# Optimization experiments

Hardware: AMD Instinct MI355X
Metric: run time of the kernel (lower is better)

Reference implementation:

```python
import jax, jax.numpy as jnp
import numpy as np

D = 256          # in_dim == out_dim for both layers
B, S = 8, 1024   # batch, seq_len
EPS = 1e-5       # LayerNorm eps (torch default)


def _layernorm(x, g, b):
    mu = jnp.mean(x, axis=-1, keepdims=True)
    var = jnp.var(x, axis=-1, keepdims=True)
    return (x - mu) * jax.lax.rsqrt(var + EPS) * g + b


def _periods(d):
    i = jnp.arange(d, dtype=jnp.float32)
    # periods[i, j] = i*d + j + 2
    return i[:, None] * d + i[None, :] + 2.0


def _layer(x, M, P, g, b, positions):
    # x: [B, S, in_dim] -> [B, S, out_dim]
    x_trans = jnp.einsum('bsj,ij->bsi', x, M)      # x @ M.T
    x_trans = _layernorm(x_trans, g, b)
    k = positions.astype(jnp.float32)[:, None, None]            # [S,1,1]
    phi = jnp.cos(2.0 * jnp.pi * k / _periods(D)[None])         # [S,D,D]
    Mk = P[None] * phi                                          # [S,D,D]
    Nk = jnp.einsum('bsj,sij->bsi', x_trans, Mk)
    # use_residual='separate' with in_dim==out_dim -> Identity residual
    return Nk + x


def setup_inputs() -> dict:
    key = jax.random.key(0)
    ks = jax.random.split(key, 5)
    seq = jax.random.normal(ks[0], (B, S, D), dtype=jnp.float32)
    M1 = jax.random.uniform(ks[1], (D, D), jnp.float32, -0.5, 0.5)
    P1 = jax.random.uniform(ks[2], (D, D), jnp.float32, -0.1, 0.1)
    M2 = jax.random.uniform(ks[3], (D, D), jnp.float32, -0.5, 0.5)
    P2 = jax.random.uniform(ks[4], (D, D), jnp.float32, -0.1, 0.1)
    g1 = jnp.ones((D,), jnp.float32); b1 = jnp.zeros((D,), jnp.float32)
    g2 = jnp.ones((D,), jnp.float32); b2 = jnp.zeros((D,), jnp.float32)
    return {"seq": seq, "M1": M1, "P1": P1, "g1": g1, "b1": b1,
            "M2": M2, "P2": P2, "g2": g2, "b2": b2}


def reference(seq, M1, P1, g1, b1, M2, P2, g2, b2):
    positions = jnp.arange(S)
    x = _layer(seq, M1, P1, g1, b1, positions)
    x = _layer(x, M2, P2, g2, b2, positions)
    return x
```

## Files before the change

### kernel.cpp

```cpp
#include <hip/hip_runtime.h>

#define DD 256
#define BB 8
#define SS 1024
#define XSTRIDE 264

#define LAYER_BYTES 524288
#define PTAB_OFF    131072
#define ITAB_OFF    262144
#define WS_NEEDED   (2 * LAYER_BYTES)

typedef _Float16 half8  __attribute__((ext_vector_type(8)));
typedef _Float16 half2t __attribute__((ext_vector_type(2)));
typedef __fp16   fp16x2 __attribute__((ext_vector_type(2)));
typedef __attribute__((ext_vector_type(4))) float float4v;

__device__ __forceinline__ half2t pkrtz(float a, float b) {
    union { fp16x2 f; half2t h; } cv;
    cv.f = __builtin_amdgcn_cvt_pkrtz(a, b);
    return cv.h;
}

__global__ void build_tabs(const float* __restrict__ M1, const float* __restrict__ P1,
                           const float* __restrict__ M2, const float* __restrict__ P2,
                           char* __restrict__ ws)
{
    int gid   = blockIdx.x * 256 + threadIdx.x;
    int layer = gid >> 13;
    int gi    = gid & 8191;
    int idx   = gi >> 6;
    int lane  = gi & 63;
    int kt    = idx >> 4;
    int wt    = idx & 15;
    int l15   = lane & 15, quad = lane >> 4;
    int n     = 16 * wt + l15;
    int j0    = kt * 32 + quad * 8;

    const float* Msrc = layer ? M2 : M1;
    const float* Psrc = layer ? P2 : P1;

    union { half8 h; half2t h2[4]; } mh, ph;
    float iv[8];
    #pragma unroll
    for (int e = 0; e < 4; ++e) {
        float ma = Msrc[(size_t)n * DD + j0 + 2 * e];
        float mb = Msrc[(size_t)n * DD + j0 + 2 * e + 1];
        float pa = Psrc[(size_t)n * DD + j0 + 2 * e];
        float pb = Psrc[(size_t)n * DD + j0 + 2 * e + 1];
        mh.h2[e] = pkrtz(ma, mb);
        ph.h2[e] = pkrtz(pa, pb);
        iv[2 * e]     = 1.0f / (float)(n * DD + j0 + 2 * e + 2);
        iv[2 * e + 1] = 1.0f / (float)(n * DD + j0 + 2 * e + 3);
    }
    char* base = ws + (size_t)layer * LAYER_BYTES;
    ((half8*)base)[gi]                       = mh.h;
    ((half8*)(base + PTAB_OFF))[gi]          = ph.h;
    float4* it = (float4*)(base + ITAB_OFF);
    it[2 * gi]     = make_float4(iv[0], iv[1], iv[2], iv[3]);
    it[2 * gi + 1] = make_float4(iv[4], iv[5], iv[6], iv[7]);
}

template<bool TABS>
__global__ __launch_bounds__(512, 4)
void fused_hierddpm(const float* __restrict__ seq,
                    const float* __restrict__ M1, const float* __restrict__ P1,
                    const float* __restrict__ g1, const float* __restrict__ be1,
                    const float* __restrict__ M2, const float* __restrict__ P2,
                    const float* __restrict__ g2, const float* __restrict__ be2,
                    const char* __restrict__ ws,
                    float* __restrict__ out)
{
    __shared__ __align__(16) _Float16 xsb[16][XSTRIDE];
    __shared__ __align__(16) _Float16 xtb[16][XSTRIDE];
    __shared__ float stats[8][16][2];

    const int tid  = threadIdx.x;
    const int w    = tid >> 6;
    const int lane = tid & 63;
    const int l15  = lane & 15;
    const int quad = lane >> 4;
    const int s0   = blockIdx.x * 2;
    const float k0 = (float)s0, k1 = (float)(s0 + 1);

    {
        const float4* seq4 = (const float4*)seq;
        #pragma unroll
        for (int u = 0; u < 2; ++u) {
            int v  = tid + 512 * u;
            int sl = v >> 9;
            int rm = v & 511;
            int b  = rm >> 6, j4 = rm & 63;
            float4 x = seq4[((size_t)b * SS + s0 + sl) * 64 + j4];
            half2t* dst = (half2t*)&xsb[sl * 8 + b][4 * j4];
            dst[0] = pkrtz(x.x, x.y);
            dst[1] = pkrtz(x.z, x.w);
        }
    }

    float res[2][4];
    {
        const int sl = quad >> 1;
        #pragma unroll
        for (int t = 0; t < 2; ++t) {
            int col = 16 * (2 * w + t) + l15;
            #pragma unroll
            for (int reg = 0; reg < 4; ++reg) {
                int b = (quad * 4 + reg) & 7;
                res[t][reg] = seq[((size_t)b * SS + s0 + sl) * DD + col];
            }
        }
    }
    __syncthreads();

    #pragma unroll 1
    for (int layer = 0; layer < 2; ++layer) {
        const float* M  = layer ? M2  : M1;
        const float* P  = layer ? P2  : P1;
        const float* g  = layer ? g2  : g1;
        const float* be = layer ? be2 : be1;
        const char*  lbase = ws + (size_t)layer * LAYER_BYTES;
        const half8*  Mtab = (const half8*)lbase;
        const half8*  Ptab = (const half8*)(lbase + PTAB_OFF);
        const float4* Itab = (const float4*)(lbase + ITAB_OFF);

        float4v acc1[2];
        acc1[0] = (float4v){0.f, 0.f, 0.f, 0.f};
        acc1[1] = (float4v){0.f, 0.f, 0.f, 0.f};

        #pragma unroll 1
        for (int kt = 0; kt < 8; ++kt) {
            half8 a = *(const half8*)&xsb[l15][kt * 32 + quad * 8];
            #pragma unroll
            for (int t = 0; t < 2; ++t) {
                half8 bfrag;
                if (TABS) {
                    bfrag = Mtab[(kt * 16 + 2 * w + t) * 64 + lane];
                } else {
                    int n = 16 * (2 * w + t) + l15;
                    const float4* Mr = (const float4*)M +
                        ((size_t)n * 64 + kt * 8 + quad * 2);
                    float4 m0 = Mr[0], m1 = Mr[1];
                    union { half8 h; half2t h2[4]; } bb;
                    bb.h2[0] = pkrtz(m0.x, m0.y);
                    bb.h2[1] = pkrtz(m0.z, m0.w);
                    bb.h2[2] = pkrtz(m1.x, m1.y);
                    bb.h2[3] = pkrtz(m1.z, m1.w);
                    bfrag = bb.h;
                }
                acc1[t] = __builtin_amdgcn_mfma_f32_16x16x32_f16(a, bfrag, acc1[t], 0, 0, 0);
            }
        }

        {
            #pragma unroll
            for (int reg = 0; reg < 4; ++reg) {
                float sm = acc1[0][reg] + acc1[1][reg];
                float sq = fmaf(acc1[0][reg], acc1[0][reg], acc1[1][reg] * acc1[1][reg]);
                #pragma unroll
                for (int off = 1; off < 16; off <<= 1) {
                    sm += __shfl_xor(sm, off, 64);
                    sq += __shfl_xor(sq, off, 64);
                }
                if (l15 == 0) {
                    stats[w][quad * 4 + reg][0] = sm;
                    stats[w][quad * 4 + reg][1] = sq;
                }
            }
        }
        __syncthreads();
        {
            float mu[4], rs[4];
            #pragma unroll
            for (int reg = 0; reg < 4; ++reg) {
                int m = quad * 4 + reg;
                float sm = 0.f, sq = 0.f;
                #pragma unroll
                for (int ww = 0; ww < 8; ++ww) {
                    sm += stats[ww][m][0];
                    sq += stats[ww][m][1];
                }
                float mm = sm * (1.f / DD);
                mu[reg] = mm;
                rs[reg] = rsqrtf(sq * (1.f / DD) - mm * mm + 1e-5f);
            }
            #pragma unroll
            for (int t = 0; t < 2; ++t) {
                int col = 16 * (2 * w + t) + l15;
                float gv = g[col], bv = be[col];
                #pragma unroll
                for (int reg = 0; reg < 4; ++reg) {
                    float v = fmaf((acc1[t][reg] - mu[reg]) * rs[reg], gv, bv);
                    xtb[quad * 4 + reg][col] = (_Float16)v;
                }
            }
        }
        __syncthreads();

        float4v accS[2][2];
        #pragma unroll
        for (int sl = 0; sl < 2; ++sl)
            #pragma unroll
            for (int t = 0; t < 2; ++t) accS[sl][t] = (float4v){0.f, 0.f, 0.f, 0.f};

        #pragma unroll 2
        for (int kt = 0; kt < 8; ++kt) {
            half8 a = *(const half8*)&xtb[l15][kt * 32 + quad * 8];
            #pragma unroll
            for (int t = 0; t < 2; ++t) {
                union { half8 h; half2t h2[4]; } pv;
                float iv[8];
                if (TABS) {
                    int gi = (kt * 16 + 2 * w + t) * 64 + lane;
                    pv.h = Ptab[gi];
                    float4 i0 = Itab[2 * gi], i1 = Itab[2 * gi + 1];
                    iv[0] = i0.x; iv[1] = i0.y; iv[2] = i0.z; iv[3] = i0.w;
                    iv[4] = i1.x; iv[5] = i1.y; iv[6] = i1.z; iv[7] = i1.w;
                } else {
                    int n = 16 * (2 * w + t) + l15;
                    const float4* Pr = (const float4*)P +
                        ((size_t)n * 64 + kt * 8 + quad * 2);
                    float4 p0 = Pr[0], p1 = Pr[1];
                    pv.h2[0] = pkrtz(p0.x, p0.y);
                    pv.h2[1] = pkrtz(p0.z, p0.w);
                    pv.h2[2] = pkrtz(p1.x, p1.y);
                    pv.h2[3] = pkrtz(p1.z, p1.w);
                    float pbase = (float)(n * DD + kt * 32 + quad * 8 + 2);
                    #pragma unroll
                    for (int e = 0; e < 8; ++e)
                        iv[e] = __builtin_amdgcn_rcpf(pbase + (float)e);
                }
                union { half8 h; half2t h2[4]; } b0, b1;
                #pragma unroll
                for (int e = 0; e < 4; ++e) {
                    float ia = iv[2 * e], ib = iv[2 * e + 1];
                    half2t c0 = pkrtz(
                        __builtin_amdgcn_cosf(__builtin_amdgcn_fractf(k0 * ia)),
                        __builtin_amdgcn_cosf(__builtin_amdgcn_fractf(k0 * ib)));
                    half2t c1 = pkrtz(
                        __builtin_amdgcn_cosf(__builtin_amdgcn_fractf(k1 * ia)),
                        __builtin_amdgcn_cosf(__builtin_amdgcn_fractf(k1 * ib)));
                    b0.h2[e] = pv.h2[e] * c0;
                    b1.h2[e] = pv.h2[e] * c1;
                }
                accS[0][t] = __builtin_amdgcn_mfma_f32_16x16x32_f16(a, b0.h, accS[0][t], 0, 0, 0);
                accS[1][t] = __builtin_amdgcn_mfma_f32_16x16x32_f16(a, b1.h, accS[1][t], 0, 0, 0);
            }
        }

        #pragma unroll
        for (int t = 0; t < 2; ++t) {
            int col = 16 * (2 * w + t) + l15;
            float4v av = (quad < 2) ? accS[0][t] : accS[1][t];
            int sl = quad >> 1;
            #pragma unroll
            for (int reg = 0; reg < 4; ++reg) {
                int m = quad * 4 + reg;
                int b = m & 7;
                float val = av[reg] + res[t][reg];
                if (layer == 0) {
                    res[t][reg] = val;
                    xsb[m][col] = (_Float16)val;
                } else {
                    out[((size_t)b * SS + s0 + sl) * DD + col] = val;
                }
            }
        }
        if (layer == 0) __syncthreads();
    }
}

extern "C" void kernel_launch(void* const* d_in, const int* in_sizes, int n_in,
                              void* d_out, int out_size, void* d_ws, size_t ws_size,
                              hipStream_t stream)
{
    const float* seq = (const float*)d_in[0];
    const float* M1  = (const float*)d_in[1];
    const float* P1  = (const float*)d_in[2];
    const float* g1  = (const float*)d_in[3];
    const float* b1  = (const float*)d_in[4];
    const float* M2  = (const float*)d_in[5];
    const float* P2  = (const float*)d_in[6];
    const float* g2  = (const float*)d_in[7];
    const float* b2  = (const float*)d_in[8];
    float* out = (float*)d_out;

    if (ws_size >= WS_NEEDED) {
        build_tabs<<<64, 256, 0, stream>>>(M1, P1, M2, P2, (char*)d_ws);
        fused_hierddpm<true><<<SS / 2, 512, 0, stream>>>(
            seq, M1, P1, g1, b1, M2, P2, g2, b2, (const char*)d_ws, out);
    } else {
        fused_hierddpm<false><<<SS / 2, 512, 0, stream>>>(
            seq, M1, P1, g1, b1, M2, P2, g2, b2, nullptr, out);
    }
}
```

Baseline: 114.0 us.

## Use 1024-thread blocks with one column tile per wave and prefetch operands

```diff
diff --git a/kernel.cpp b/kernel.cpp
--- a/kernel.cpp
+++ b/kernel.cpp
@@ -61,7 +61,7 @@
 }
 
 template<bool TABS>
-__global__ __launch_bounds__(512, 4)
+__global__ __launch_bounds__(1024, 8)
 void fused_hierddpm(const float* __restrict__ seq,
                     const float* __restrict__ M1, const float* __restrict__ P1,
                     const float* __restrict__ g1, const float* __restrict__ be1,
@@ -72,7 +72,7 @@
 {
     __shared__ __align__(16) _Float16 xsb[16][XSTRIDE];
     __shared__ __align__(16) _Float16 xtb[16][XSTRIDE];
-    __shared__ float stats[8][16][2];
+    __shared__ float2 stats[16][16];
 
     const int tid  = threadIdx.x;
     const int w    = tid >> 6;
@@ -81,34 +81,24 @@
     const int quad = lane >> 4;
     const int s0   = blockIdx.x * 2;
     const float k0 = (float)s0, k1 = (float)(s0 + 1);
+    const int col  = 16 * w + l15;
 
     {
         const float4* seq4 = (const float4*)seq;
-        #pragma unroll
-        for (int u = 0; u < 2; ++u) {
-            int v  = tid + 512 * u;
-            int sl = v >> 9;
-            int rm = v & 511;
-            int b  = rm >> 6, j4 = rm & 63;
-            float4 x = seq4[((size_t)b * SS + s0 + sl) * 64 + j4];
-            half2t* dst = (half2t*)&xsb[sl * 8 + b][4 * j4];
-            dst[0] = pkrtz(x.x, x.y);
-            dst[1] = pkrtz(x.z, x.w);
-        }
-    }
-
-    float res[2][4];
-    {
-        const int sl = quad >> 1;
-        #pragma unroll
-        for (int t = 0; t < 2; ++t) {
-            int col = 16 * (2 * w + t) + l15;
-            #pragma unroll
-            for (int reg = 0; reg < 4; ++reg) {
-                int b = (quad * 4 + reg) & 7;
-                res[t][reg] = seq[((size_t)b * SS + s0 + sl) * DD + col];
-            }
-        }
+        int sl = tid >> 9;
+        int rm = tid & 511;
+        int b  = rm >> 6, j4 = rm & 63;
+        float4 x = seq4[((size_t)b * SS + s0 + sl) * 64 + j4];
+        half2t* dst = (half2t*)&xsb[sl * 8 + b][4 * j4];
+        dst[0] = pkrtz(x.x, x.y);
+        dst[1] = pkrtz(x.z, x.w);
+    }
+
+    float res[4];
+    #pragma unroll
+    for (int reg = 0; reg < 4; ++reg) {
+        int m = quad * 4 + reg;
+        res[reg] = seq[((size_t)(m & 7) * SS + s0 + (m >> 3)) * DD + col];
     }
     __syncthreads();
 
@@ -123,111 +113,85 @@
         const half8*  Ptab = (const half8*)(lbase + PTAB_OFF);
         const float4* Itab = (const float4*)(lbase + ITAB_OFF);
 
-        float4v acc1[2];
-        acc1[0] = (float4v){0.f, 0.f, 0.f, 0.f};
-        acc1[1] = (float4v){0.f, 0.f, 0.f, 0.f};
-
-        #pragma unroll 1
-        for (int kt = 0; kt < 8; ++kt) {
-            half8 a = *(const half8*)&xsb[l15][kt * 32 + quad * 8];
+        float4v acc1 = (float4v){0.f, 0.f, 0.f, 0.f};
+
+        if (TABS) {
+            half8 aN = *(const half8*)&xsb[l15][quad * 8];
+            half8 bN = Mtab[w * 64 + lane];
+            #pragma unroll 1
+            for (int kt = 0; kt < 8; ++kt) {
+                half8 aC = aN, bC = bN;
+                if (kt < 7) {
+                    aN = *(const half8*)&xsb[l15][(kt + 1) * 32 + quad * 8];
+                    bN = Mtab[((kt + 1) * 16 + w) * 64 + lane];
+                }
+                acc1 = __builtin_amdgcn_mfma_f32_16x16x32_f16(aC, bC, acc1, 0, 0, 0);
+            }
+        } else {
+            #pragma unroll 1
+            for (int kt = 0; kt < 8; ++kt) {
+                half8 a = *(const half8*)&xsb[l15][kt * 32 + quad * 8];
+                int n = 16 * w + l15;
+                const float4* Mr = (const float4*)M + ((size_t)n * 64 + kt * 8 + quad * 2);
+                float4 m0 = Mr[0], m1 = Mr[1];
+                union { half8 h; half2t h2[4]; } bb2;
+                bb2.h2[0] = pkrtz(m0.x, m0.y);
+                bb2.h2[1] = pkrtz(m0.z, m0.w);
+                bb2.h2[2] = pkrtz(m1.x, m1.y);
+                bb2.h2[3] = pkrtz(m1.z, m1.w);
+                acc1 = __builtin_amdgcn_mfma_f32_16x16x32_f16(a, bb2.h, acc1, 0, 0, 0);
+            }
+        }
+
+        #pragma unroll
+        for (int reg = 0; reg < 4; ++reg) {
+            float sm = acc1[reg];
+            float sq = acc1[reg] * acc1[reg];
             #pragma unroll
-            for (int t = 0; t < 2; ++t) {
-                half8 bfrag;
-                if (TABS) {
-                    bfrag = Mtab[(kt * 16 + 2 * w + t) * 64 + lane];
-                } else {
-                    int n = 16 * (2 * w + t) + l15;
-                    const float4* Mr = (const float4*)M +
-                        ((size_t)n * 64 + kt * 8 + quad * 2);
-                    float4 m0 = Mr[0], m1 = Mr[1];
-                    union { half8 h; half2t h2[4]; } bb;
-                    bb.h2[0] = pkrtz(m0.x, m0.y);
-                    bb.h2[1] = pkrtz(m0.z, m0.w);
-                    bb.h2[2] = pkrtz(m1.x, m1.y);
-                    bb.h2[3] = pkrtz(m1.z, m1.w);
-                    bfrag = bb.h;
-                }
-                acc1[t] = __builtin_amdgcn_mfma_f32_16x16x32_f16(a, bfrag, acc1[t], 0, 0, 0);
-            }
-        }
-
-        {
-            #pragma unroll
-            for (int reg = 0; reg < 4; ++reg) {
-                float sm = acc1[0][reg] + acc1[1][reg];
-                float sq = fmaf(acc1[0][reg], acc1[0][reg], acc1[1][reg] * acc1[1][reg]);
-                #pragma unroll
-                for (int off = 1; off < 16; off <<= 1) {
-                    sm += __shfl_xor(sm, off, 64);
-                    sq += __shfl_xor(sq, off, 64);
-                }
-                if (l15 == 0) {
-                    stats[w][quad * 4 + reg][0] = sm;
-                    stats[w][quad * 4 + reg][1] = sq;
-                }
-            }
+            for (int off = 1; off < 16; off <<= 1) {
+                sm += __shfl_xor(sm, off, 64);
+                sq += __shfl_xor(sq, off, 64);
+            }
+            if (l15 == 0) stats[w][quad * 4 + reg] = make_float2(sm, sq);
         }
         __syncthreads();
         {
-            float mu[4], rs[4];
+            float gv = g[col], bv = be[col];
             #pragma unroll
             for (int reg = 0; reg < 4; ++reg) {
                 int m = quad * 4 + reg;
                 float sm = 0.f, sq = 0.f;
                 #pragma unroll
-                for (int ww = 0; ww < 8; ++ww) {
-                    sm += stats[ww][m][0];
-                    sq += stats[ww][m][1];
+                for (int ww = 0; ww < 16; ++ww) {
+                    float2 v = stats[ww][m];
+                    sm += v.x; sq += v.y;
                 }
                 float mm = sm * (1.f / DD);
-                mu[reg] = mm;
-                rs[reg] = rsqrtf(sq * (1.f / DD) - mm * mm + 1e-5f);
-            }
-            #pragma unroll
-            for (int t = 0; t < 2; ++t) {
-                int col = 16 * (2 * w + t) + l15;
-                float gv = g[col], bv = be[col];
-                #pragma unroll
-                for (int reg = 0; reg < 4; ++reg) {
-                    float v = fmaf((acc1[t][reg] - mu[reg]) * rs[reg], gv, bv);
-                    xtb[quad * 4 + reg][col] = (_Float16)v;
-                }
+                float rs = rsqrtf(sq * (1.f / DD) - mm * mm + 1e-5f);
+                xtb[m][col] = (_Float16)fmaf((acc1[reg] - mm) * rs, gv, bv);
             }
         }
         __syncthreads();
 
-        float4v accS[2][2];
-        #pragma unroll
-        for (int sl = 0; sl < 2; ++sl)
-            #pragma unroll
-            for (int t = 0; t < 2; ++t) accS[sl][t] = (float4v){0.f, 0.f, 0.f, 0.f};
-
-        #pragma unroll 2
-        for (int kt = 0; kt < 8; ++kt) {
-            half8 a = *(const half8*)&xtb[l15][kt * 32 + quad * 8];
-            #pragma unroll
-            for (int t = 0; t < 2; ++t) {
-                union { half8 h; half2t h2[4]; } pv;
-                float iv[8];
-                if (TABS) {
-                    int gi = (kt * 16 + 2 * w + t) * 64 + lane;
-                    pv.h = Ptab[gi];
-                    float4 i0 = Itab[2 * gi], i1 = Itab[2 * gi + 1];
-                    iv[0] = i0.x; iv[1] = i0.y; iv[2] = i0.z; iv[3] = i0.w;
-                    iv[4] = i1.x; iv[5] = i1.y; iv[6] = i1.z; iv[7] = i1.w;
-                } else {
-                    int n = 16 * (2 * w + t) + l15;
-                    const float4* Pr = (const float4*)P +
-                        ((size_t)n * 64 + kt * 8 + quad * 2);
-                    float4 p0 = Pr[0], p1 = Pr[1];
-                    pv.h2[0] = pkrtz(p0.x, p0.y);
-                    pv.h2[1] = pkrtz(p0.z, p0.w);
-                    pv.h2[2] = pkrtz(p1.x, p1.y);
-                    pv.h2[3] = pkrtz(p1.z, p1.w);
-                    float pbase = (float)(n * DD + kt * 32 + quad * 8 + 2);
-                    #pragma unroll
-                    for (int e = 0; e < 8; ++e)
-                        iv[e] = __builtin_amdgcn_rcpf(pbase + (float)e);
+        float4v accS0 = (float4v){0.f, 0.f, 0.f, 0.f};
+        float4v accS1 = (float4v){0.f, 0.f, 0.f, 0.f};
+
+        if (TABS) {
+            int gi0 = w * 64 + lane;
+            half8 aN = *(const half8*)&xtb[l15][quad * 8];
+            half8 pN = Ptab[gi0];
+            float4 iN0 = Itab[2 * gi0], iN1 = Itab[2 * gi0 + 1];
+            #pragma unroll 1
+            for (int kt = 0; kt < 8; ++kt) {
+                half8 aC = aN;
+                union { half8 h; half2t h2[4]; } pv; pv.h = pN;
+                float iv[8] = {iN0.x, iN0.y, iN0.z, iN0.w, iN1.x, iN1.y, iN1.z, iN1.w};
+                if (kt < 7) {
+                    int gin = ((kt + 1) * 16 + w) * 64 + lane;
+                    aN  = *(const half8*)&xtb[l15][(kt + 1) * 32 + quad * 8];
+                    pN  = Ptab[gin];
+                    iN0 = Itab[2 * gin];
+                    iN1 = Itab[2 * gin + 1];
                 }
                 union { half8 h; half2t h2[4]; } b0, b1;
                 #pragma unroll
@@ -242,27 +206,50 @@
                     b0.h2[e] = pv.h2[e] * c0;
                     b1.h2[e] = pv.h2[e] * c1;
                 }
-                accS[0][t] = __builtin_amdgcn_mfma_f32_16x16x32_f16(a, b0.h, accS[0][t], 0, 0, 0);
-                accS[1][t] = __builtin_amdgcn_mfma_f32_16x16x32_f16(a, b1.h, accS[1][t], 0, 0, 0);
+                accS0 = __builtin_amdgcn_mfma_f32_16x16x32_f16(aC, b0.h, accS0, 0, 0, 0);
+                accS1 = __builtin_amdgcn_mfma_f32_16x16x32_f16(aC, b1.h, accS1, 0, 0, 0);
+            }
+        } else {
+            #pragma unroll 1
+            for (int kt = 0; kt < 8; ++kt) {
+                half8 a = *(const half8*)&xtb[l15][kt * 32 + quad * 8];
+                int n = 16 * w + l15;
+                const float4* Pr = (const float4*)P + ((size_t)n * 64 + kt * 8 + quad * 2);
+                float4 p0 = Pr[0], p1 = Pr[1];
+                union { half8 h; half2t h2[4]; } pv;
+                pv.h2[0] = pkrtz(p0.x, p0.y);
+                pv.h2[1] = pkrtz(p0.z, p0.w);
+                pv.h2[2] = pkrtz(p1.x, p1.y);
+                pv.h2[3] = pkrtz(p1.z, p1.w);
+                float pbase = (float)(n * DD + kt * 32 + quad * 8 + 2);
+                union { half8 h; half2t h2[4]; } b0, b1;
+                #pragma unroll
+                for (int e = 0; e < 4; ++e) {
+                    float ia = __builtin_amdgcn_rcpf(pbase + (float)(2 * e));
+                    float ib = __builtin_amdgcn_rcpf(pbase + (float)(2 * e + 1));
+                    half2t c0 = pkrtz(
+                        __builtin_amdgcn_cosf(__builtin_amdgcn_fractf(k0 * ia)),
+                        __builtin_amdgcn_cosf(__builtin_amdgcn_fractf(k0 * ib)));
+                    half2t c1 = pkrtz(
+                        __builtin_amdgcn_cosf(__builtin_amdgcn_fractf(k1 * ia)),
+                        __builtin_amdgcn_cosf(__builtin_amdgcn_fractf(k1 * ib)));
+                    b0.h2[e] = pv.h2[e] * c0;
+                    b1.h2[e] = pv.h2[e] * c1;
+                }
+                accS0 = __builtin_amdgcn_mfma_f32_16x16x32_f16(a, b0.h, accS0, 0, 0, 0);
+                accS1 = __builtin_amdgcn_mfma_f32_16x16x32_f16(a, b1.h, accS1, 0, 0, 0);
             }
         }
 
         #pragma unroll
-        for (int t = 0; t < 2; ++t) {
-            int col = 16 * (2 * w + t) + l15;
-            float4v av = (quad < 2) ? accS[0][t] : accS[1][t];
-            int sl = quad >> 1;
-            #pragma unroll
-            for (int reg = 0; reg < 4; ++reg) {
-                int m = quad * 4 + reg;
-                int b = m & 7;
-                float val = av[reg] + res[t][reg];
-                if (layer == 0) {
-                    res[t][reg] = val;
-                    xsb[m][col] = (_Float16)val;
-                } else {
-                    out[((size_t)b * SS + s0 + sl) * DD + col] = val;
-                }
+        for (int reg = 0; reg < 4; ++reg) {
+            int m = quad * 4 + reg;
+            float av = ((quad < 2) ? accS0[reg] : accS1[reg]) + res[reg];
+            if (layer == 0) {
+                res[reg] = av;
+                xsb[m][col] = (_Float16)av;
+            } else {
+                out[((size_t)(m & 7) * SS + s0 + (m >> 3)) * DD + col] = av;
             }
         }
         if (layer == 0) __syncthreads();
@@ -286,10 +273,10 @@
 
     if (ws_size >= WS_NEEDED) {
         build_tabs<<<64, 256, 0, stream>>>(M1, P1, M2, P2, (char*)d_ws);
-        fused_hierddpm<true><<<SS / 2, 512, 0, stream>>>(
+        fused_hierddpm<true><<<SS / 2, 1024, 0, stream>>>(
             seq, M1, P1, g1, b1, M2, P2, g2, b2, (const char*)d_ws, out);
     } else {
-        fused_hierddpm<false><<<SS / 2, 512, 0, stream>>>(
+        fused_hierddpm<false><<<SS / 2, 1024, 0, stream>>>(
             seq, M1, P1, g1, b1, M2, P2, g2, b2, nullptr, out);
     }
 }
```

Measured after the change: 177.8 us. +56.0%, slower.

## Split batch across two blocks per position pair and recompute reciprocal periods inline

Applied to the files above, without the earlier changes.

```diff
diff --git a/kernel.cpp b/kernel.cpp
--- a/kernel.cpp
+++ b/kernel.cpp
@@ -5,9 +5,8 @@
 #define SS 1024
 #define XSTRIDE 264
 
-#define LAYER_BYTES 524288
+#define LAYER_BYTES 262144
 #define PTAB_OFF    131072
-#define ITAB_OFF    262144
 #define WS_NEEDED   (2 * LAYER_BYTES)
 
 typedef _Float16 half8  __attribute__((ext_vector_type(8)));
@@ -30,9 +29,9 @@
     int gi    = gid & 8191;
     int idx   = gi >> 6;
     int lane  = gi & 63;
-    int kt    = idx >> 4;
     int wt    = idx & 15;
     int l15   = lane & 15, quad = lane >> 4;
+    int kt    = idx >> 4;
     int n     = 16 * wt + l15;
     int j0    = kt * 32 + quad * 8;
 
@@ -40,7 +39,6 @@
     const float* Psrc = layer ? P2 : P1;
 
     union { half8 h; half2t h2[4]; } mh, ph;
-    float iv[8];
     #pragma unroll
     for (int e = 0; e < 4; ++e) {
         float ma = Msrc[(size_t)n * DD + j0 + 2 * e];
@@ -49,19 +47,14 @@
         float pb = Psrc[(size_t)n * DD + j0 + 2 * e + 1];
         mh.h2[e] = pkrtz(ma, mb);
         ph.h2[e] = pkrtz(pa, pb);
-        iv[2 * e]     = 1.0f / (float)(n * DD + j0 + 2 * e + 2);
-        iv[2 * e + 1] = 1.0f / (float)(n * DD + j0 + 2 * e + 3);
     }
     char* base = ws + (size_t)layer * LAYER_BYTES;
-    ((half8*)base)[gi]                       = mh.h;
-    ((half8*)(base + PTAB_OFF))[gi]          = ph.h;
-    float4* it = (float4*)(base + ITAB_OFF);
-    it[2 * gi]     = make_float4(iv[0], iv[1], iv[2], iv[3]);
-    it[2 * gi + 1] = make_float4(iv[4], iv[5], iv[6], iv[7]);
+    ((half8*)base)[gi]              = mh.h;
+    ((half8*)(base + PTAB_OFF))[gi] = ph.h;
 }
 
 template<bool TABS>
-__global__ __launch_bounds__(512, 4)
+__global__ __launch_bounds__(512, 6)
 void fused_hierddpm(const float* __restrict__ seq,
                     const float* __restrict__ M1, const float* __restrict__ P1,
                     const float* __restrict__ g1, const float* __restrict__ be1,
@@ -72,42 +65,38 @@
 {
     __shared__ __align__(16) _Float16 xsb[16][XSTRIDE];
     __shared__ __align__(16) _Float16 xtb[16][XSTRIDE];
-    __shared__ float stats[8][16][2];
+    __shared__ __align__(16) float2 stats[8][8];
 
     const int tid  = threadIdx.x;
     const int w    = tid >> 6;
     const int lane = tid & 63;
     const int l15  = lane & 15;
     const int quad = lane >> 4;
-    const int s0   = blockIdx.x * 2;
+    const int sp   = blockIdx.x >> 1;
+    const int bh   = blockIdx.x & 1;
+    const int s0   = sp * 2;
     const float k0 = (float)s0, k1 = (float)(s0 + 1);
 
     {
         const float4* seq4 = (const float4*)seq;
-        #pragma unroll
-        for (int u = 0; u < 2; ++u) {
-            int v  = tid + 512 * u;
-            int sl = v >> 9;
-            int rm = v & 511;
-            int b  = rm >> 6, j4 = rm & 63;
-            float4 x = seq4[((size_t)b * SS + s0 + sl) * 64 + j4];
-            half2t* dst = (half2t*)&xsb[sl * 8 + b][4 * j4];
-            dst[0] = pkrtz(x.x, x.y);
-            dst[1] = pkrtz(x.z, x.w);
-        }
-    }
-
-    float res[2][4];
-    {
-        const int sl = quad >> 1;
+        int r  = tid >> 6;
+        int j4 = tid & 63;
+        int b  = bh * 4 + (r & 3);
+        int sl = r >> 2;
+        float4 x = seq4[((size_t)b * SS + s0 + sl) * 64 + j4];
+        half2t* dst = (half2t*)&xsb[r][4 * j4];
+        dst[0] = pkrtz(x.x, x.y);
+        dst[1] = pkrtz(x.z, x.w);
+    }
+
+    float res[2][4] = {};
+    if (quad < 2) {
         #pragma unroll
         for (int t = 0; t < 2; ++t) {
             int col = 16 * (2 * w + t) + l15;
             #pragma unroll
-            for (int reg = 0; reg < 4; ++reg) {
-                int b = (quad * 4 + reg) & 7;
-                res[t][reg] = seq[((size_t)b * SS + s0 + sl) * DD + col];
-            }
+            for (int reg = 0; reg < 4; ++reg)
+                res[t][reg] = seq[((size_t)(bh * 4 + reg) * SS + s0 + quad) * DD + col];
         }
     }
     __syncthreads();
@@ -119,15 +108,14 @@
         const float* g  = layer ? g2  : g1;
         const float* be = layer ? be2 : be1;
         const char*  lbase = ws + (size_t)layer * LAYER_BYTES;
-        const half8*  Mtab = (const half8*)lbase;
-        const half8*  Ptab = (const half8*)(lbase + PTAB_OFF);
-        const float4* Itab = (const float4*)(lbase + ITAB_OFF);
+        const half8* Mtab = (const half8*)lbase;
+        const half8* Ptab = (const half8*)(lbase + PTAB_OFF);
 
         float4v acc1[2];
         acc1[0] = (float4v){0.f, 0.f, 0.f, 0.f};
         acc1[1] = (float4v){0.f, 0.f, 0.f, 0.f};
 
-        #pragma unroll 1
+        #pragma unroll 2
         for (int kt = 0; kt < 8; ++kt) {
             half8 a = *(const half8*)&xsb[l15][kt * 32 + quad * 8];
             #pragma unroll
@@ -140,83 +128,77 @@
                     const float4* Mr = (const float4*)M +
                         ((size_t)n * 64 + kt * 8 + quad * 2);
                     float4 m0 = Mr[0], m1 = Mr[1];
-                    union { half8 h; half2t h2[4]; } bb;
-                    bb.h2[0] = pkrtz(m0.x, m0.y);
-                    bb.h2[1] = pkrtz(m0.z, m0.w);
-                    bb.h2[2] = pkrtz(m1.x, m1.y);
-                    bb.h2[3] = pkrtz(m1.z, m1.w);
-                    bfrag = bb.h;
+                    union { half8 h; half2t h2[4]; } bb2;
+                    bb2.h2[0] = pkrtz(m0.x, m0.y);
+                    bb2.h2[1] = pkrtz(m0.z, m0.w);
+                    bb2.h2[2] = pkrtz(m1.x, m1.y);
+                    bb2.h2[3] = pkrtz(m1.z, m1.w);
+                    bfrag = bb2.h;
                 }
                 acc1[t] = __builtin_amdgcn_mfma_f32_16x16x32_f16(a, bfrag, acc1[t], 0, 0, 0);
             }
         }
 
-        {
-            #pragma unroll
-            for (int reg = 0; reg < 4; ++reg) {
-                float sm = acc1[0][reg] + acc1[1][reg];
-                float sq = fmaf(acc1[0][reg], acc1[0][reg], acc1[1][reg] * acc1[1][reg]);
-                #pragma unroll
-                for (int off = 1; off < 16; off <<= 1) {
-                    sm += __shfl_xor(sm, off, 64);
-                    sq += __shfl_xor(sq, off, 64);
-                }
-                if (l15 == 0) {
-                    stats[w][quad * 4 + reg][0] = sm;
-                    stats[w][quad * 4 + reg][1] = sq;
-                }
-            }
+        #pragma unroll
+        for (int reg = 0; reg < 4; ++reg) {
+            float v0 = acc1[0][reg], v1 = acc1[1][reg];
+            float sm = v0 + v1;
+            float sq = fmaf(v0, v0, v1 * v1);
+            #pragma unroll
+            for (int off = 1; off < 16; off <<= 1) {
+                sm += __shfl_xor(sm, off, 64);
+                sq += __shfl_xor(sq, off, 64);
+            }
+            if (l15 == 0 && quad < 2) stats[quad * 4 + reg][w] = make_float2(sm, sq);
         }
         __syncthreads();
-        {
-            float mu[4], rs[4];
+        if (quad < 2) {
+            float gv[2], bv[2];
+            #pragma unroll
+            for (int t = 0; t < 2; ++t) {
+                int col = 16 * (2 * w + t) + l15;
+                gv[t] = g[col]; bv[t] = be[col];
+            }
             #pragma unroll
             for (int reg = 0; reg < 4; ++reg) {
                 int m = quad * 4 + reg;
-                float sm = 0.f, sq = 0.f;
-                #pragma unroll
-                for (int ww = 0; ww < 8; ++ww) {
-                    sm += stats[ww][m][0];
-                    sq += stats[ww][m][1];
-                }
+                const float4* sp4 = (const float4*)&stats[m][0];
+                float4 q0 = sp4[0], q1 = sp4[1], q2 = sp4[2], q3 = sp4[3];
+                float sm = (q0.x + q0.z) + (q1.x + q1.z) + (q2.x + q2.z) + (q3.x + q3.z);
+                float sq = (q0.y + q0.w) + (q1.y + q1.w) + (q2.y + q2.w) + (q3.y + q3.w);
                 float mm = sm * (1.f / DD);
-                mu[reg] = mm;
-                rs[reg] = rsqrtf(sq * (1.f / DD) - mm * mm + 1e-5f);
-            }
-            #pragma unroll
-            for (int t = 0; t < 2; ++t) {
-                int col = 16 * (2 * w + t) + l15;
-                float gv = g[col], bv = be[col];
-                #pragma unroll
-                for (int reg = 0; reg < 4; ++reg) {
-                    float v = fmaf((acc1[t][reg] - mu[reg]) * rs[reg], gv, bv);
-                    xtb[quad * 4 + reg][col] = (_Float16)v;
-                }
-            }
+                float rs = rsqrtf(sq * (1.f / DD) - mm * mm + 1e-5f);
+                #pragma unroll
+                for (int t = 0; t < 2; ++t) {
+                    int col = 16 * (2 * w + t) + l15;
+                    xtb[m][col] = (_Float16)fmaf((acc1[t][reg] - mm) * rs, gv[t], bv[t]);
+                }
+            }
+        } else {
+            #pragma unroll
+            for (int reg = 0; reg < 4; ++reg)
+                #pragma unroll
+                for (int t = 0; t < 2; ++t)
+                    xtb[quad * 4 + reg][16 * (2 * w + t) + l15] = (_Float16)0.f;
         }
         __syncthreads();
 
         float4v accS[2][2];
         #pragma unroll
-        for (int sl = 0; sl < 2; ++sl)
-            #pragma unroll
-            for (int t = 0; t < 2; ++t) accS[sl][t] = (float4v){0.f, 0.f, 0.f, 0.f};
+        for (int k = 0; k < 2; ++k)
+            #pragma unroll
+            for (int t = 0; t < 2; ++t) accS[k][t] = (float4v){0.f, 0.f, 0.f, 0.f};
 
         #pragma unroll 2
         for (int kt = 0; kt < 8; ++kt) {
             half8 a = *(const half8*)&xtb[l15][kt * 32 + quad * 8];
             #pragma unroll
             for (int t = 0; t < 2; ++t) {
+                int n = 16 * (2 * w + t) + l15;
                 union { half8 h; half2t h2[4]; } pv;
-                float iv[8];
                 if (TABS) {
-                    int gi = (kt * 16 + 2 * w + t) * 64 + lane;
-                    pv.h = Ptab[gi];
-                    float4 i0 = Itab[2 * gi], i1 = Itab[2 * gi + 1];
-                    iv[0] = i0.x; iv[1] = i0.y; iv[2] = i0.z; iv[3] = i0.w;
-                    iv[4] = i1.x; iv[5] = i1.y; iv[6] = i1.z; iv[7] = i1.w;
+                    pv.h = Ptab[(kt * 16 + 2 * w + t) * 64 + lane];
                 } else {
-                    int n = 16 * (2 * w + t) + l15;
                     const float4* Pr = (const float4*)P +
                         ((size_t)n * 64 + kt * 8 + quad * 2);
                     float4 p0 = Pr[0], p1 = Pr[1];
@@ -224,15 +206,13 @@
                     pv.h2[1] = pkrtz(p0.z, p0.w);
                     pv.h2[2] = pkrtz(p1.x, p1.y);
                     pv.h2[3] = pkrtz(p1.z, p1.w);
-                    float pbase = (float)(n * DD + kt * 32 + quad * 8 + 2);
-                    #pragma unroll
-                    for (int e = 0; e < 8; ++e)
-                        iv[e] = __builtin_amdgcn_rcpf(pbase + (float)e);
-                }
+                }
+                float pbase = (float)(n * DD + kt * 32 + quad * 8 + 2);
                 union { half8 h; half2t h2[4]; } b0, b1;
                 #pragma unroll
                 for (int e = 0; e < 4; ++e) {
-                    float ia = iv[2 * e], ib = iv[2 * e + 1];
+                    float ia = __builtin_amdgcn_rcpf(pbase + (float)(2 * e));
+                    float ib = __builtin_amdgcn_rcpf(pbase + (float)(2 * e + 1));
                     half2t c0 = pkrtz(
                         __builtin_amdgcn_cosf(__builtin_amdgcn_fractf(k0 * ia)),
                         __builtin_amdgcn_cosf(__builtin_amdgcn_fractf(k0 * ib)));
@@ -247,21 +227,21 @@
             }
         }
 
-        #pragma unroll
-        for (int t = 0; t < 2; ++t) {
-            int col = 16 * (2 * w + t) + l15;
-            float4v av = (quad < 2) ? accS[0][t] : accS[1][t];
-            int sl = quad >> 1;
-            #pragma unroll
-            for (int reg = 0; reg < 4; ++reg) {
-                int m = quad * 4 + reg;
-                int b = m & 7;
-                float val = av[reg] + res[t][reg];
-                if (layer == 0) {
-                    res[t][reg] = val;
-                    xsb[m][col] = (_Float16)val;
-                } else {
-                    out[((size_t)b * SS + s0 + sl) * DD + col] = val;
+        if (quad < 2) {
+            #pragma unroll
+            for (int t = 0; t < 2; ++t) {
+                int col = 16 * (2 * w + t) + l15;
+                float4v av = (quad == 0) ? accS[0][t] : accS[1][t];
+                #pragma unroll
+                for (int reg = 0; reg < 4; ++reg) {
+                    int m = quad * 4 + reg;
+                    float val = av[reg] + res[t][reg];
+                    if (layer == 0) {
+                        res[t][reg] = val;
+                        xsb[m][col] = (_Float16)val;
+                    } else {
+                        out[((size_t)(bh * 4 + reg) * SS + s0 + quad) * DD + col] = val;
+                    }
                 }
             }
         }
@@ -286,10 +266,10 @@
 
     if (ws_size >= WS_NEEDED) {
         build_tabs<<<64, 256, 0, stream>>>(M1, P1, M2, P2, (char*)d_ws);
-        fused_hierddpm<true><<<SS / 2, 512, 0, stream>>>(
+        fused_hierddpm<true><<<SS, 512, 0, stream>>>(
             seq, M1, P1, g1, b1, M2, P2, g2, b2, (const char*)d_ws, out);
     } else {
-        fused_hierddpm<false><<<SS / 2, 512, 0, stream>>>(
+        fused_hierddpm<false><<<SS, 512, 0, stream>>>(
             seq, M1, P1, g1, b1, M2, P2, g2, b2, nullptr, out);
     }
 }
```

New measurement: 147.6 us. 29.5% more time.
